# Kernel tuning notes

Hardware: AMD Instinct MI355X
Metric: run time of the kernel (lower is better)

## Reference

```python
import jax, jax.numpy as jnp
import numpy as np

B, F, E, H = 4096, 26, 64, 1000000
D = F * E  # 1664

def setup_inputs() -> dict:
    key = jax.random.key(0)
    ks = jax.random.split(key, 12)
    s = 0.02  # init scale
    return {
        "ids": jax.random.randint(ks[0], (B, F), 0, H),
        "emb": jax.random.normal(ks[1], (H, E), jnp.float32) * s,
        "cross_w": jax.random.normal(ks[2], (3, D), jnp.float32) * s,
        "cross_b": jnp.zeros((3, D), jnp.float32),
        "w1": jax.random.normal(ks[3], (D, 1024), jnp.float32) * s,
        "b1": jnp.zeros((1024,), jnp.float32),
        "w2": jax.random.normal(ks[4], (1024, 512), jnp.float32) * s,
        "b2": jnp.zeros((512,), jnp.float32),
        "w3": jax.random.normal(ks[5], (512, 256), jnp.float32) * s,
        "b3": jnp.zeros((256,), jnp.float32),
        "out_w": jax.random.normal(ks[6], (D + 256, 1), jnp.float32) * s,
        "out_b": jnp.zeros((), jnp.float32),
    }

def reference(ids, emb, cross_w, cross_b, w1, b1, w2, b2, w3, b3, out_w, out_b):
    # Embedding lookup + field-wise concat -> x0: [B, D]
    x0 = emb[ids].reshape(ids.shape[0], -1)
    # Cross net. Original materializes [B,D,D] outer product x0 * x^T then
    # giving the same math with O(B*D) memory.
    x = x0
    for i in range(cross_w.shape[0]):
        s = x @ cross_w[i]                 # [B] per-example scalar
        x = x0 * s[:, None] + cross_b[i] + x
    # Deep tower on x0
    h = jax.nn.relu(x0 @ w1 + b1)
    h = jax.nn.relu(h @ w2 + b2)
    h = jax.nn.relu(h @ w3 + b3)
    # Output head
    logit = jnp.concatenate([x, h], axis=1) @ out_w + out_b  # [B, 1]
    return jax.nn.sigmoid(logit)
```

## Files before the change

### kernel.cpp

```cpp
#include <hip/hip_runtime.h>
#include <hip/hip_bf16.h>

#define B_  4096
#define F_  26
#define E_  64
#define D_  1664
#define N1_ 1024
#define N2_ 512
#define N3_ 256

typedef __attribute__((ext_vector_type(8))) __bf16 bf16x8;
typedef __attribute__((ext_vector_type(4))) float  f32x4;

__device__ __forceinline__ unsigned short f2b(float x) {
    __hip_bfloat16 h = __float2bfloat16(x);
    return __builtin_bit_cast(unsigned short, h);
}
__device__ __forceinline__ float b2f(unsigned short u) {
    return __uint_as_float(((unsigned)u) << 16);
}

__device__ __forceinline__ void async_load16(const void* g, void* l) {
    __builtin_amdgcn_global_load_lds(
        (const __attribute__((address_space(1))) void*)g,
        (__attribute__((address_space(3))) void*)l,
        16, 0, 0);
}

__device__ __forceinline__ f32x4 mfma16(bf16x8 a, bf16x8 b, f32x4 c) {
    return __builtin_amdgcn_mfma_f32_16x16x32_bf16(a, b, c, 0, 0, 0);
}

__global__ __launch_bounds__(256) void gather_cross_kernel(
        const int* __restrict__ ids, const float* __restrict__ emb,
        const float* __restrict__ cw, const float* __restrict__ cb,
        const float* __restrict__ out_w,
        unsigned short* __restrict__ x0b, float* __restrict__ partial)
{
    __shared__ int   sid[F_];
    __shared__ float red[4];
    const int b = blockIdx.x;
    const int t = threadIdx.x;
    const int lane = t & 63, w = t >> 6;

    if (t < F_) sid[t] = ids[b * F_ + t];
    __syncthreads();

    float x0r[7], xv[7];
    #pragma unroll
    for (int j = 0; j < 7; j++) {
        const int d = t + j * 256;
        float v = 0.f;
        if (d < D_) {
            const int f = d >> 6;
            v = emb[(size_t)sid[f] * E_ + (d & 63)];
            x0b[(size_t)b * D_ + d] = f2b(v);
        }
        x0r[j] = v; xv[j] = v;
    }
    for (int i = 0; i < 3; i++) {
        float s = 0.f;
        #pragma unroll
        for (int j = 0; j < 7; j++) {
            const int d = t + j * 256;
            if (d < D_) s += xv[j] * cw[i * D_ + d];
        }
        #pragma unroll
        for (int off = 32; off > 0; off >>= 1) s += __shfl_down(s, off, 64);
        __syncthreads();
        if (lane == 0) red[w] = s;
        __syncthreads();
        const float st = red[0] + red[1] + red[2] + red[3];
        #pragma unroll
        for (int j = 0; j < 7; j++) {
            const int d = t + j * 256;
            if (d < D_) xv[j] = x0r[j] * st + cb[i * D_ + d] + xv[j];
        }
    }
    float s = 0.f;
    #pragma unroll
    for (int j = 0; j < 7; j++) {
        const int d = t + j * 256;
        if (d < D_) s += xv[j] * out_w[d];
    }
    #pragma unroll
    for (int off = 32; off > 0; off >>= 1) s += __shfl_down(s, off, 64);
    __syncthreads();
    if (lane == 0) red[w] = s;
    __syncthreads();
    if (t == 0) partial[b] = red[0] + red[1] + red[2] + red[3];
}

__global__ __launch_bounds__(256) void transpose_cast_kernel(
        const float* __restrict__ in, unsigned short* __restrict__ out,
        int K, int N)
{
    __shared__ float tile[32][33];
    const int n0 = blockIdx.x * 32, k0 = blockIdx.y * 32;
    const int tc = threadIdx.x & 31, tr = threadIdx.x >> 5;
    #pragma unroll
    for (int p = 0; p < 4; p++)
        tile[tr + p * 8][tc] = in[(size_t)(k0 + tr + p * 8) * N + n0 + tc];
    __syncthreads();
    #pragma unroll
    for (int p = 0; p < 4; p++) {
        const int n = tr + p * 8;
        out[(size_t)(n0 + n) * K + k0 + tc] = f2b(tile[tc][n]);
    }
}

template<int BM, int BN>
__global__ __launch_bounds__(256, 4) void gemm_bias_relu(
        const unsigned short* __restrict__ A,
        const unsigned short* __restrict__ Bt,
        const float* __restrict__ bias,
        unsigned short* __restrict__ C,
        int M, int N, int K)
{
    constexpr int WM = BM / 2, WN = BN / 2;
    constexpr int TI = WM / 16, TJ = WN / 16;
    constexpr int nA = BM / 16, nB = BN / 16, nAB = nA + nB;
    constexpr int TOTC = 2 * nAB;

    __shared__ unsigned short sA[2 * BM * 32];
    __shared__ unsigned short sB[2 * BN * 32];

    const int t    = threadIdx.x;
    const int lane = t & 63;
    const int w    = t >> 6;

    const int i    = blockIdx.y * gridDim.x + blockIdx.x;
    const int xcd  = i & 7;
    const int s    = i >> 3;
    const int ypg  = gridDim.y >> 3;
    const int ty   = xcd * ypg + s / gridDim.x;
    const int tx   = s - (s / gridDim.x) * gridDim.x;
    const int m0   = ty * BM;
    const int n0   = tx * BN;
    const int wm   = (w >> 1) * WM;
    const int wn   = (w & 1) * WN;

    const int srow = lane >> 2;
    const int scol = (lane & 3) * 8;

    f32x4 acc[TI][TJ] = {};

    for (int k0 = 0; k0 < K; k0 += 64) {
        #pragma unroll
        for (int c0 = 0; c0 < TOTC; c0 += 4) {
            const int c = c0 + w;
            const int u = c / nAB;
            const int r = c - u * nAB;
            if (r < nA) {
                const unsigned short* g =
                    A + (size_t)(m0 + r * 16 + srow) * K + k0 + u * 32 + scol;
                async_load16(g, &sA[u * BM * 32 + r * 512]);
            } else {
                const int rb = r - nA;
                const unsigned short* g =
                    Bt + (size_t)(n0 + rb * 16 + srow) * K + k0 + u * 32 + scol;
                async_load16(g, &sB[u * BN * 32 + rb * 512]);
            }
        }
        __syncthreads();

        #pragma unroll
        for (int u = 0; u < 2; u++) {
            bf16x8 af[TI], bf[TJ];
            #pragma unroll
            for (int ii = 0; ii < TI; ii++)
                af[ii] = *(const bf16x8*)
                    &sA[u * BM * 32 + (wm + ii * 16 + (lane & 15)) * 32 + (lane >> 4) * 8];
            #pragma unroll
            for (int j = 0; j < TJ; j++)
                bf[j] = *(const bf16x8*)
                    &sB[u * BN * 32 + (wn + j * 16 + (lane & 15)) * 32 + (lane >> 4) * 8];
            #pragma unroll
            for (int ii = 0; ii < TI; ii++)
                #pragma unroll
                for (int j = 0; j < TJ; j++)
                    acc[ii][j] = mfma16(af[ii], bf[j], acc[ii][j]);
        }
        __syncthreads();
    }

    #pragma unroll
    for (int ii = 0; ii < TI; ii++) {
        const int r0 = m0 + wm + ii * 16 + (lane >> 4) * 4;
        #pragma unroll
        for (int j = 0; j < TJ; j++) {
            const int col = n0 + wn + j * 16 + (lane & 15);
            const float bv = bias[col];
            #pragma unroll
            for (int r = 0; r < 4; r++) {
                float v = acc[ii][j][r] + bv;
                v = fmaxf(v, 0.f);
                C[(size_t)(r0 + r) * N + col] = f2b(v);
            }
        }
    }
}

__global__ __launch_bounds__(256) void head_kernel(
        const float* __restrict__ partial, const unsigned short* __restrict__ h3,
        const float* __restrict__ out_w, const float* __restrict__ out_b,
        float* __restrict__ out)
{
    const int gw   = (blockIdx.x * 256 + threadIdx.x) >> 6;
    const int lane = threadIdx.x & 63;
    if (gw >= B_) return;
    float s = 0.f;
    #pragma unroll
    for (int q = 0; q < 4; q++) {
        const int j = lane + q * 64;
        s += b2f(h3[(size_t)gw * N3_ + j]) * out_w[D_ + j];
    }
    #pragma unroll
    for (int off = 32; off > 0; off >>= 1) s += __shfl_down(s, off, 64);
    if (lane == 0) {
        const float logit = partial[gw] + s + out_b[0];
        out[gw] = 1.f / (1.f + expf(-logit));
    }
}

extern "C" void kernel_launch(void* const* d_in, const int* in_sizes, int n_in,
                              void* d_out, int out_size, void* d_ws, size_t ws_size,
                              hipStream_t stream)
{
    (void)in_sizes; (void)n_in; (void)out_size; (void)ws_size;
    const int*   ids     = (const int*)  d_in[0];
    const float* emb     = (const float*)d_in[1];
    const float* cross_w = (const float*)d_in[2];
    const float* cross_b = (const float*)d_in[3];
    const float* w1      = (const float*)d_in[4];
    const float* b1      = (const float*)d_in[5];
    const float* w2      = (const float*)d_in[6];
    const float* b2      = (const float*)d_in[7];
    const float* w3      = (const float*)d_in[8];
    const float* b3      = (const float*)d_in[9];
    const float* out_w   = (const float*)d_in[10];
    const float* out_b   = (const float*)d_in[11];
    float* out = (float*)d_out;

    char* p = (char*)d_ws;
    auto alloc = [&](size_t bytes) {
        char* r = p; p += (bytes + 255) & ~(size_t)255; return r;
    };
    unsigned short* x0b = (unsigned short*)alloc((size_t)B_ * D_ * 2);
    unsigned short* w1t = (unsigned short*)alloc((size_t)D_ * N1_ * 2);
    unsigned short* w2t = (unsigned short*)alloc((size_t)N1_ * N2_ * 2);
    unsigned short* w3t = (unsigned short*)alloc((size_t)N2_ * N3_ * 2);
    unsigned short* h1  = (unsigned short*)alloc((size_t)B_ * N1_ * 2);
    unsigned short* h2  = (unsigned short*)alloc((size_t)B_ * N2_ * 2);
    unsigned short* h3  = (unsigned short*)alloc((size_t)B_ * N3_ * 2);
    float* partial      = (float*)alloc((size_t)B_ * 4);

    gather_cross_kernel<<<B_, 256, 0, stream>>>(
        ids, emb, cross_w, cross_b, out_w, x0b, partial);
    transpose_cast_kernel<<<dim3(N1_ / 32, D_  / 32), 256, 0, stream>>>(w1, w1t, D_,  N1_);
    transpose_cast_kernel<<<dim3(N2_ / 32, N1_ / 32), 256, 0, stream>>>(w2, w2t, N1_, N2_);
    transpose_cast_kernel<<<dim3(N3_ / 32, N2_ / 32), 256, 0, stream>>>(w3, w3t, N2_, N3_);

    gemm_bias_relu<64, 64><<<dim3(N1_ / 64, B_ / 64), 256, 0, stream>>>(
        x0b, w1t, b1, h1, B_, N1_, D_);
    gemm_bias_relu<64, 32><<<dim3(N2_ / 32, B_ / 64), 256, 0, stream>>>(
        h1, w2t, b2, h2, B_, N2_, N1_);
    gemm_bias_relu<32, 32><<<dim3(N3_ / 32, B_ / 32), 256, 0, stream>>>(
        h2, w3t, b3, h3, B_, N3_, N2_);

    head_kernel<<<B_ / 4, 256, 0, stream>>>(partial, h3, out_w, out_b, out);
}
```

Measured before the change: 385.9 us.

## Vectorize gather, merge weight transposes, and double GEMM K-chunk per barrier

The gather/cross kernel now uses float4 loads for embeddings and cross weights and writes bf16 as ushort4, reducing instruction count and memory transactions. The three weight-transpose launches are merged into one kernel that picks its matrix from the block index, saving launch overhead. The GEMM template gains a K-chunk parameter set to 128, halving the number of synchronisation barriers per K loop at the cost of double the LDS per block, which may reduce occupancy.

```diff
diff --git a/kernel.cpp b/kernel.cpp
--- a/kernel.cpp
+++ b/kernel.cpp
@@ -35,35 +35,46 @@
         const int* __restrict__ ids, const float* __restrict__ emb,
         const float* __restrict__ cw, const float* __restrict__ cb,
         const float* __restrict__ out_w,
-        unsigned short* __restrict__ x0b, float* __restrict__ partial)
+        unsigned short* __restrict__ x0out, float* __restrict__ partial)
 {
     __shared__ int   sid[F_];
     __shared__ float red[4];
     const int b = blockIdx.x;
     const int t = threadIdx.x;
     const int lane = t & 63, w = t >> 6;
+    constexpr int C4 = D_ / 4;
 
     if (t < F_) sid[t] = ids[b * F_ + t];
     __syncthreads();
 
-    float x0r[7], xv[7];
-    #pragma unroll
-    for (int j = 0; j < 7; j++) {
-        const int d = t + j * 256;
-        float v = 0.f;
-        if (d < D_) {
-            const int f = d >> 6;
-            v = emb[(size_t)sid[f] * E_ + (d & 63)];
-            x0b[(size_t)b * D_ + d] = f2b(v);
-        }
-        x0r[j] = v; xv[j] = v;
+    const float4* emb4 = (const float4*)emb;
+    const float4* cw4  = (const float4*)cw;
+    const float4* cb4  = (const float4*)cb;
+    const float4* ow4  = (const float4*)out_w;
+
+    float4 x0v[2], xv[2];
+    #pragma unroll
+    for (int j = 0; j < 2; j++) {
+        const int c = t + j * 256;
+        float4 v = make_float4(0.f, 0.f, 0.f, 0.f);
+        if (c < C4) {
+            const int f = c >> 4;
+            v = emb4[(size_t)sid[f] * 16 + (c & 15)];
+            ushort4 o;
+            o.x = f2b(v.x); o.y = f2b(v.y); o.z = f2b(v.z); o.w = f2b(v.w);
+            ((ushort4*)x0out)[(size_t)b * C4 + c] = o;
+        }
+        x0v[j] = v; xv[j] = v;
     }
     for (int i = 0; i < 3; i++) {
         float s = 0.f;
         #pragma unroll
-        for (int j = 0; j < 7; j++) {
-            const int d = t + j * 256;
-            if (d < D_) s += xv[j] * cw[i * D_ + d];
+        for (int j = 0; j < 2; j++) {
+            const int c = t + j * 256;
+            if (c < C4) {
+                const float4 wv = cw4[i * C4 + c];
+                s += xv[j].x * wv.x + xv[j].y * wv.y + xv[j].z * wv.z + xv[j].w * wv.w;
+            }
         }
         #pragma unroll
         for (int off = 32; off > 0; off >>= 1) s += __shfl_down(s, off, 64);
@@ -72,16 +83,25 @@
         __syncthreads();
         const float st = red[0] + red[1] + red[2] + red[3];
         #pragma unroll
-        for (int j = 0; j < 7; j++) {
-            const int d = t + j * 256;
-            if (d < D_) xv[j] = x0r[j] * st + cb[i * D_ + d] + xv[j];
+        for (int j = 0; j < 2; j++) {
+            const int c = t + j * 256;
+            if (c < C4) {
+                const float4 bv = cb4[i * C4 + c];
+                xv[j].x = x0v[j].x * st + bv.x + xv[j].x;
+                xv[j].y = x0v[j].y * st + bv.y + xv[j].y;
+                xv[j].z = x0v[j].z * st + bv.z + xv[j].z;
+                xv[j].w = x0v[j].w * st + bv.w + xv[j].w;
+            }
         }
     }
     float s = 0.f;
     #pragma unroll
-    for (int j = 0; j < 7; j++) {
-        const int d = t + j * 256;
-        if (d < D_) s += xv[j] * out_w[d];
+    for (int j = 0; j < 2; j++) {
+        const int c = t + j * 256;
+        if (c < C4) {
+            const float4 wv = ow4[c];
+            s += xv[j].x * wv.x + xv[j].y * wv.y + xv[j].z * wv.z + xv[j].w * wv.w;
+        }
     }
     #pragma unroll
     for (int off = 32; off > 0; off >>= 1) s += __shfl_down(s, off, 64);
@@ -91,12 +111,21 @@
     if (t == 0) partial[b] = red[0] + red[1] + red[2] + red[3];
 }
 
-__global__ __launch_bounds__(256) void transpose_cast_kernel(
-        const float* __restrict__ in, unsigned short* __restrict__ out,
-        int K, int N)
+__global__ __launch_bounds__(256) void transpose_all_kernel(
+        const float* __restrict__ w1, const float* __restrict__ w2,
+        const float* __restrict__ w3,
+        unsigned short* __restrict__ o1, unsigned short* __restrict__ o2,
+        unsigned short* __restrict__ o3)
 {
     __shared__ float tile[32][33];
-    const int n0 = blockIdx.x * 32, k0 = blockIdx.y * 32;
+    const int bid = blockIdx.x;
+    const float* in; unsigned short* out; int K, N, lg, t0;
+    if (bid < 1664)      { in = w1; out = o1; K = D_;  N = N1_; lg = 5; t0 = 0;    }
+    else if (bid < 2176) { in = w2; out = o2; K = N1_; N = N2_; lg = 4; t0 = 1664; }
+    else                 { in = w3; out = o3; K = N2_; N = N3_; lg = 3; t0 = 2176; }
+    const int tl = bid - t0;
+    const int n0 = (tl & ((1 << lg) - 1)) * 32;
+    const int k0 = (tl >> lg) * 32;
     const int tc = threadIdx.x & 31, tr = threadIdx.x >> 5;
     #pragma unroll
     for (int p = 0; p < 4; p++)
@@ -109,7 +138,7 @@
     }
 }
 
-template<int BM, int BN>
+template<int BM, int BN, int BKC>
 __global__ __launch_bounds__(256, 4) void gemm_bias_relu(
         const unsigned short* __restrict__ A,
         const unsigned short* __restrict__ Bt,
@@ -117,13 +146,14 @@
         unsigned short* __restrict__ C,
         int M, int N, int K)
 {
+    constexpr int KU = BKC / 32;
     constexpr int WM = BM / 2, WN = BN / 2;
     constexpr int TI = WM / 16, TJ = WN / 16;
     constexpr int nA = BM / 16, nB = BN / 16, nAB = nA + nB;
-    constexpr int TOTC = 2 * nAB;
-
-    __shared__ unsigned short sA[2 * BM * 32];
-    __shared__ unsigned short sB[2 * BN * 32];
+    constexpr int TOTC = KU * nAB;
+
+    __shared__ unsigned short sA[KU * BM * 32];
+    __shared__ unsigned short sB[KU * BN * 32];
 
     const int t    = threadIdx.x;
     const int lane = t & 63;
@@ -145,7 +175,7 @@
 
     f32x4 acc[TI][TJ] = {};
 
-    for (int k0 = 0; k0 < K; k0 += 64) {
+    for (int k0 = 0; k0 < K; k0 += BKC) {
         #pragma unroll
         for (int c0 = 0; c0 < TOTC; c0 += 4) {
             const int c = c0 + w;
@@ -165,7 +195,7 @@
         __syncthreads();
 
         #pragma unroll
-        for (int u = 0; u < 2; u++) {
+        for (int u = 0; u < KU; u++) {
             bf16x8 af[TI], bf[TJ];
             #pragma unroll
             for (int ii = 0; ii < TI; ii++)
@@ -257,15 +287,13 @@
 
     gather_cross_kernel<<<B_, 256, 0, stream>>>(
         ids, emb, cross_w, cross_b, out_w, x0b, partial);
-    transpose_cast_kernel<<<dim3(N1_ / 32, D_  / 32), 256, 0, stream>>>(w1, w1t, D_,  N1_);
-    transpose_cast_kernel<<<dim3(N2_ / 32, N1_ / 32), 256, 0, stream>>>(w2, w2t, N1_, N2_);
-    transpose_cast_kernel<<<dim3(N3_ / 32, N2_ / 32), 256, 0, stream>>>(w3, w3t, N2_, N3_);
-
-    gemm_bias_relu<64, 64><<<dim3(N1_ / 64, B_ / 64), 256, 0, stream>>>(
+    transpose_all_kernel<<<2304, 256, 0, stream>>>(w1, w2, w3, w1t, w2t, w3t);
+
+    gemm_bias_relu<64, 64, 128><<<dim3(N1_ / 64, B_ / 64), 256, 0, stream>>>(
         x0b, w1t, b1, h1, B_, N1_, D_);
-    gemm_bias_relu<64, 32><<<dim3(N2_ / 32, B_ / 64), 256, 0, stream>>>(
+    gemm_bias_relu<64, 32, 128><<<dim3(N2_ / 32, B_ / 64), 256, 0, stream>>>(
         h1, w2t, b2, h2, B_, N2_, N1_);
-    gemm_bias_relu<32, 32><<<dim3(N3_ / 32, B_ / 32), 256, 0, stream>>>(
+    gemm_bias_relu<32, 32, 128><<<dim3(N3_ / 32, B_ / 32), 256, 0, stream>>>(
         h2, w3t, b3, h3, B_, N3_, N2_);
 
     head_kernel<<<B_ / 4, 256, 0, stream>>>(partial, h3, out_w, out_b, out);
```

Result: no change. 380.4 us (-1.4%).
